# Kernel optimization log

Hardware: AMD Instinct MI355X
Metric: run time of the kernel (lower is better)

The kernel has to match this reference:

```python
import jax, jax.numpy as jnp
import numpy as np

N_UNITS = 100
N_INPUTS = 7
N_OUTPUTS = 1
T = 60
STIM_ON, STIM_OFF = 10, 15
RESP_START, RESP_END = 20, 35
REWARD_DURATION = 5
ALPHA = 0.2            # dt / tau = 100 / 500
SIGMA_REC = 0.15
B = 8192


def setup_inputs() -> dict:
    key = jax.random.key(0)
    k1, k2, k3, k4, k5, k6, k7 = jax.random.split(key, 7)
    W_in_raw = (jax.random.normal(k1, (N_UNITS, N_INPUTS)) * 0.05).astype(jnp.float32)
    W_rec_np = np.asarray(jax.random.normal(k2, (N_UNITS, N_UNITS))) / np.sqrt(N_UNITS)
    sr = float(np.abs(np.linalg.eigvals(W_rec_np)).max())
    W_rec = jnp.asarray(W_rec_np * (0.8 / sr), dtype=jnp.float32)
    b_rec = jnp.zeros((N_UNITS,), jnp.float32)
    w_out = (jax.random.normal(k3, (N_OUTPUTS, N_UNITS)) * 0.1).astype(jnp.float32)
    b_out = jnp.zeros((N_OUTPUTS,), jnp.float32)
    return {
        "y0": jnp.zeros((B, N_UNITS), jnp.float32),
        "noise": jax.random.normal(k4, (B, T, N_UNITS), dtype=jnp.float32),
        "stimulus_idx": jax.random.randint(k5, (B,), 0, 4).astype(jnp.int32),
        "rewarded_target_idx": jax.random.randint(k6, (B,), 0, 4).astype(jnp.int32),
        "instruction": jax.random.randint(k7, (B,), 0, 2).astype(jnp.int32),
        "W_in_raw": W_in_raw, "W_rec": W_rec, "b_rec": b_rec,
        "w_out": w_out, "b_out": b_out,
    }


def reference(y0, noise, stimulus_idx, rewarded_target_idx, instruction,
              W_in_raw, W_rec, b_rec, w_out, b_out):
    W_in = jnp.abs(W_in_raw)               # [N, n_in]
    w_lick = W_in[:, 5]
    w_reward = W_in[:, 4]
    noise_scale = SIGMA_REC * float(np.sqrt(2.0 * ALPHA))
    t_idx = jnp.arange(T, dtype=jnp.int32)
    stim_mask = ((t_idx >= STIM_ON) & (t_idx < STIM_OFF)).astype(jnp.float32)
    resp_mask = ((t_idx >= RESP_START) & (t_idx < RESP_END)).astype(jnp.float32)
    auto_start = RESP_END - REWARD_DURATION

    def trial(y0_i, eps_i, stim, rew, instr):
        is_rew = stim == rew
        instr_b = instr > 0
        # base open-loop input: stimulus channel + response cue (channel 6)
        u_base = jnp.zeros((T, N_INPUTS), jnp.float32).at[:, 6].set(resp_mask)
        u_base = u_base + stim_mask[:, None] * jax.nn.one_hot(stim, N_INPUTS, dtype=jnp.float32)
        wu = u_base @ W_in.T + b_rec        # [T, N]

        def step(carry, xs):
            y, licked, lick_t, instr_fired = carry
            t, wu_t, eps_t = xs
            # instruction auto-reward fires at auto_start if no reward yet (applied BEFORE pre)
            delivered = instr_fired | (licked & is_rew)
            fire = instr_b & (~delivered) & (t == auto_start)
            instr_fired = instr_fired | fire
            instr_active = instr_fired & (t >= auto_start) & (t < RESP_END)
            # lick-triggered inputs affect dynamics only AFTER the lick step (wu[t] already consumed)
            lick_dyn = licked & (t > lick_t) & (t < lick_t + REWARD_DURATION)
            add = (instr_active.astype(jnp.float32) + (lick_dyn & is_rew).astype(jnp.float32)) * w_reward \
                  + lick_dyn.astype(jnp.float32) * w_lick
            pre = y @ W_rec.T + wu_t + add + noise_scale * eps_t
            y = (1.0 - ALPHA) * y + ALPHA * jax.nn.relu(pre)
            z = jax.nn.sigmoid(y @ w_out.T + b_out)[0]
            # closed-loop lick decision (after readout)
            in_resp = (t >= RESP_START) & (t < RESP_END)
            trig = in_resp & (~licked) & (z > 0.5)
            lick_t = jnp.where(trig, t, lick_t)
            licked = licked | trig
            # u_trial markings include the lick step itself
            u5 = licked & (t >= lick_t) & (t < lick_t + REWARD_DURATION)
            u4 = instr_active | (u5 & is_rew)
            return (y, licked, lick_t, instr_fired), (z, u5, u4)

        init = (y0_i, jnp.array(False), jnp.array(T + 1, jnp.int32), jnp.array(False))
        (yf, licked, lick_t, instr_fired), (z_seq, u5, u4) = jax.lax.scan(
            step, init, (t_idx, wu, eps_i))
        u = u_base.at[:, 5].set(u5.astype(jnp.float32)).at[:, 4].set(u4.astype(jnp.float32))
        reward_delivered = instr_fired | (licked & is_rew)
        target = jnp.where(is_rew, resp_mask, jnp.zeros_like(resp_mask))
        return u, target, resp_mask > 0, licked, reward_delivered, z_seq, yf

    return jax.vmap(trial)(y0, noise, stimulus_idx, rewarded_target_idx, instruction)
```

## Files before the change

kernel.cpp:

```cpp
#include <hip/hip_runtime.h>
#include <math.h>

#define BB 8192
#define TT 60
#define NU 100
#define NI 7

typedef float v2f __attribute__((ext_vector_type(2)));

#define FOR50(M) M(0) M(1) M(2) M(3) M(4) M(5) M(6) M(7) M(8) M(9) \
  M(10) M(11) M(12) M(13) M(14) M(15) M(16) M(17) M(18) M(19) \
  M(20) M(21) M(22) M(23) M(24) M(25) M(26) M(27) M(28) M(29) \
  M(30) M(31) M(32) M(33) M(34) M(35) M(36) M(37) M(38) M(39) \
  M(40) M(41) M(42) M(43) M(44) M(45) M(46) M(47) M(48) M(49)

#define DECLW(sl) \
  const v2f wA_##sl = { W_rec[uao + 2*(sl)],     W_rec[ubo + 2*(sl)]     }; \
  const v2f wB_##sl = { W_rec[uao + 2*(sl) + 1], W_rec[ubo + 2*(sl) + 1] };

#define RL(v,l) __int_as_float(__builtin_amdgcn_readlane(__float_as_int(v), l))

#define MAC(sl) { \
  const float ya = RL(yy.x, sl); \
  const float yb = RL(yy.y, sl); \
  if ((sl) & 1) { accB0 += ya * wA_##sl; accB1 += yb * wB_##sl; } \
  else          { accA0 += ya * wA_##sl; accA1 += yb * wB_##sl; } }

#define DPPADD(ctrl, rmask) { \
  const int _t = __builtin_amdgcn_update_dpp(0, __float_as_int(part), (ctrl), (rmask), 0xf, false); \
  part += __int_as_float(_t); }

__global__ __launch_bounds__(256, 1)
void drr_kernel(const float* __restrict__ y0,
                const float* __restrict__ noise,
                const int*   __restrict__ stim_idx,
                const int*   __restrict__ rew_idx,
                const int*   __restrict__ instr_in,
                const float* __restrict__ W_in_raw,
                const float* __restrict__ W_rec,
                const float* __restrict__ b_rec,
                const float* __restrict__ w_out,
                const float* __restrict__ b_out,
                float* __restrict__ out)
{
    const int lane  = threadIdx.x & 63;
    const int wid   = threadIdx.x >> 6;
    const int trial = blockIdx.x * 4 + wid;

    const bool act = (lane < 50);
    const int  la  = act ? lane : 49;
    const int  ua  = 2 * la;
    const int  uao = ua * NU;
    const int  ubo = uao + NU;

    const int  stim    = stim_idx[trial];
    const int  rew     = rew_idx[trial];
    const bool is_rew  = (stim == rew);
    const bool instr_b = (instr_in[trial] > 0);

    FOR50(DECLW)

    const v2f wi6 = { fabsf(W_in_raw[ua * NI + 6]),    fabsf(W_in_raw[(ua+1) * NI + 6]) };
    const v2f wis = { fabsf(W_in_raw[ua * NI + stim]), fabsf(W_in_raw[(ua+1) * NI + stim]) };
    const v2f wr  = { fabsf(W_in_raw[ua * NI + 4]),    fabsf(W_in_raw[(ua+1) * NI + 4]) };
    const v2f wl  = { fabsf(W_in_raw[ua * NI + 5]),    fabsf(W_in_raw[(ua+1) * NI + 5]) };
    const v2f br  = { b_rec[ua], b_rec[ua + 1] };
    const v2f wo  = act ? (v2f){ w_out[ua], w_out[ua + 1] } : (v2f){ 0.0f, 0.0f };
    const float bo = b_out[0];

    const v2f* y0v = (const v2f*)(y0 + trial * NU);
    v2f yy = y0v[la];

    const float NS = 0.09486832980505138f;

    bool licked = false, instr_fired = false;
    int  lick_t = TT + 1;

    const float* nbase = noise + trial * (TT * NU);
    v2f en = ((const v2f*)nbase)[la];

    float* uout  = out;
    float* tout  = out  + BB * TT * NI;
    float* rout  = tout + BB * TT;
    float* lout  = rout + BB * TT;
    float* dout  = lout + BB;
    float* zout  = dout + BB;
    float* yfout = zout + BB * TT;

    for (int t = 0; t < TT; ++t) {
        const v2f e = en;
        if (t < TT - 1)
            en = ((const v2f*)(nbase + (t + 1) * NU))[la];

        const float sm = (t >= 10 && t < 15) ? 1.0f : 0.0f;
        const float rm = (t >= 20 && t < 35) ? 1.0f : 0.0f;

        const bool delivered    = instr_fired || (licked && is_rew);
        const bool fire         = instr_b && !delivered && (t == 30);
        instr_fired             = instr_fired || fire;
        const bool instr_active = instr_fired && (t >= 30) && (t < 35);
        const bool lick_dyn     = licked && (t > lick_t) && (t < lick_t + 5);
        const float a_rew  = (instr_active ? 1.0f : 0.0f) + ((lick_dyn && is_rew) ? 1.0f : 0.0f);
        const float a_lick = lick_dyn ? 1.0f : 0.0f;

        v2f accA0 = br + rm * wi6 + sm * wis + a_rew * wr + a_lick * wl + NS * e;
        v2f accA1 = { 0.0f, 0.0f };
        v2f accB0 = { 0.0f, 0.0f };
        v2f accB1 = { 0.0f, 0.0f };

        FOR50(MAC)

        const v2f pre = (accA0 + accA1) + (accB0 + accB1);
        const v2f prer = { fmaxf(pre.x, 0.0f), fmaxf(pre.y, 0.0f) };
        yy = 0.8f * yy + 0.2f * prer;

        float part = yy.x * wo.x + yy.y * wo.y;
        DPPADD(0x111, 0xf)
        DPPADD(0x112, 0xf)
        DPPADD(0x114, 0xf)
        DPPADD(0x118, 0xf)
        DPPADD(0x142, 0xa)
        DPPADD(0x143, 0xc)
        const float x = RL(part, 63) + bo;
        const float z = 1.0f / (1.0f + expf(-x));

        const bool in_resp = (t >= 20) && (t < 35);
        const bool trig    = in_resp && !licked && (z > 0.5f);
        if (trig) lick_t = t;
        licked = licked || trig;
        const bool u5 = licked && (t >= lick_t) && (t < lick_t + 5);
        const bool u4 = instr_active || (u5 && is_rew);

        const int bt = trial * TT + t;
        if (lane < NI) {
            float uv = 0.0f;
            if (lane == stim) uv = sm;
            if (lane == 4)    uv = u4 ? 1.0f : 0.0f;
            if (lane == 5)    uv = u5 ? 1.0f : 0.0f;
            if (lane == 6)    uv = rm;
            uout[bt * NI + lane] = uv;
        } else if (lane == 8) {
            tout[bt] = is_rew ? rm : 0.0f;
        } else if (lane == 9) {
            rout[bt] = rm;
        } else if (lane == 10) {
            zout[bt] = z;
        }
    }

    if (lane == 0) {
        lout[trial] = licked ? 1.0f : 0.0f;
        dout[trial] = (instr_fired || (licked && is_rew)) ? 1.0f : 0.0f;
    }
    if (act)
        ((v2f*)(yfout + trial * NU))[la] = yy;
}

extern "C" void kernel_launch(void* const* d_in, const int* in_sizes, int n_in,
                              void* d_out, int out_size, void* d_ws, size_t ws_size,
                              hipStream_t stream) {
    const float* y0       = (const float*)d_in[0];
    const float* noise    = (const float*)d_in[1];
    const int*   stim     = (const int*)  d_in[2];
    const int*   rew      = (const int*)  d_in[3];
    const int*   instr    = (const int*)  d_in[4];
    const float* W_in_raw = (const float*)d_in[5];
    const float* W_rec    = (const float*)d_in[6];
    const float* b_rec    = (const float*)d_in[7];
    const float* w_out    = (const float*)d_in[8];
    const float* b_out    = (const float*)d_in[9];
    float* out = (float*)d_out;

    drr_kernel<<<BB / 4, 256, 0, stream>>>(y0, noise, stim, rew, instr,
                                           W_in_raw, W_rec, b_rec, w_out, b_out, out);
}
```

Measured before the change: 585.8 us.

## Split recurrent matvec across block waves via LDS partial sums

Each of the four waves in a block now holds a 28-column slice of W_rec and computes partial matvec contributions for all four trials in the block, reading hidden states from LDS instead of broadcasting them with readlane. Partial sums are exchanged through LDS and combined by the owning wave, with two block-wide barriers per timestep. This cuts the per-thread weight register footprint so launch bounds can allow three blocks per CU, trading readlane-serialised work for LDS traffic and synchronisation.

```diff
diff --git a/kernel.cpp b/kernel.cpp
--- a/kernel.cpp
+++ b/kernel.cpp
@@ -7,30 +7,17 @@
 #define NI 7
 
 typedef float v2f __attribute__((ext_vector_type(2)));
-
-#define FOR50(M) M(0) M(1) M(2) M(3) M(4) M(5) M(6) M(7) M(8) M(9) \
-  M(10) M(11) M(12) M(13) M(14) M(15) M(16) M(17) M(18) M(19) \
-  M(20) M(21) M(22) M(23) M(24) M(25) M(26) M(27) M(28) M(29) \
-  M(30) M(31) M(32) M(33) M(34) M(35) M(36) M(37) M(38) M(39) \
-  M(40) M(41) M(42) M(43) M(44) M(45) M(46) M(47) M(48) M(49)
-
-#define DECLW(sl) \
-  const v2f wA_##sl = { W_rec[uao + 2*(sl)],     W_rec[ubo + 2*(sl)]     }; \
-  const v2f wB_##sl = { W_rec[uao + 2*(sl) + 1], W_rec[ubo + 2*(sl) + 1] };
-
+typedef float v4f __attribute__((ext_vector_type(4)));
+
+
+#define KEEP(x) asm volatile("" : "+v"(x))
 #define RL(v,l) __int_as_float(__builtin_amdgcn_readlane(__float_as_int(v), l))
-
-#define MAC(sl) { \
-  const float ya = RL(yy.x, sl); \
-  const float yb = RL(yy.y, sl); \
-  if ((sl) & 1) { accB0 += ya * wA_##sl; accB1 += yb * wB_##sl; } \
-  else          { accA0 += ya * wA_##sl; accA1 += yb * wB_##sl; } }
 
 #define DPPADD(ctrl, rmask) { \
   const int _t = __builtin_amdgcn_update_dpp(0, __float_as_int(part), (ctrl), (rmask), 0xf, false); \
   part += __int_as_float(_t); }
 
-__global__ __launch_bounds__(256, 1)
+__global__ __launch_bounds__(256, 3)
 void drr_kernel(const float* __restrict__ y0,
                 const float* __restrict__ noise,
                 const int*   __restrict__ stim_idx,
@@ -46,19 +33,31 @@
     const int lane  = threadIdx.x & 63;
     const int wid   = threadIdx.x >> 6;
     const int trial = blockIdx.x * 4 + wid;
+    const int kc    = wid * 28;
 
     const bool act = (lane < 50);
     const int  la  = act ? lane : 49;
     const int  ua  = 2 * la;
     const int  uao = ua * NU;
-    const int  ubo = uao + NU;
-
-    const int  stim    = stim_idx[trial];
-    const int  rew     = rew_idx[trial];
-    const bool is_rew  = (stim == rew);
-    const bool instr_b = (instr_in[trial] > 0);
-
-    FOR50(DECLW)
+
+    const int  stim   = stim_idx[trial];
+    const bool isrew  = (stim == rew_idx[trial]);
+    const bool instrb = (instr_in[trial] > 0);
+
+    v2f wa[14], wb[14];
+#pragma unroll
+    for (int p = 0; p < 14; ++p) {
+        const int k = kc + 2 * p;
+        if (k < NU) {
+            wa[p] = *(const v2f*)(W_rec + uao + k);
+            wb[p] = *(const v2f*)(W_rec + uao + NU + k);
+        } else {
+            wa[p] = (v2f){0.0f, 0.0f};
+            wb[p] = (v2f){0.0f, 0.0f};
+        }
+    }
+#pragma unroll
+    for (int p = 0; p < 14; ++p) { KEEP(wa[p]); KEEP(wb[p]); }
 
     const v2f wi6 = { fabsf(W_in_raw[ua * NI + 6]),    fabsf(W_in_raw[(ua+1) * NI + 6]) };
     const v2f wis = { fabsf(W_in_raw[ua * NI + stim]), fabsf(W_in_raw[(ua+1) * NI + stim]) };
@@ -68,16 +67,22 @@
     const v2f wo  = act ? (v2f){ w_out[ua], w_out[ua + 1] } : (v2f){ 0.0f, 0.0f };
     const float bo = b_out[0];
 
-    const v2f* y0v = (const v2f*)(y0 + trial * NU);
-    v2f yy = y0v[la];
+    v2f yy = ((const v2f*)(y0 + trial * NU))[la];
 
     const float NS = 0.09486832980505138f;
 
-    bool licked = false, instr_fired = false;
-    int  lick_t = TT + 1;
+    bool licked = false, fired = false;
+    int  lickt = TT + 1;
 
     const float* nbase = noise + trial * (TT * NU);
     v2f en = ((const v2f*)nbase)[la];
+
+    __shared__ v4f lds_y[4][28];
+    __shared__ v2f lds_p[4][4][64];
+
+    if (lane < 56)
+        ((v2f*)&lds_y[wid][0])[lane] = act ? yy : (v2f){0.0f, 0.0f};
+    __syncthreads();
 
     float* uout  = out;
     float* tout  = out  + BB * TT * NI;
@@ -87,32 +92,65 @@
     float* zout  = dout + BB;
     float* yfout = zout + BB * TT;
 
+    const v4f* Y0 = (const v4f*)&lds_y[0][0] + (kc >> 2);
+    const v4f* Y1 = (const v4f*)&lds_y[1][0] + (kc >> 2);
+    const v4f* Y2 = (const v4f*)&lds_y[2][0] + (kc >> 2);
+    const v4f* Y3 = (const v4f*)&lds_y[3][0] + (kc >> 2);
+
     for (int t = 0; t < TT; ++t) {
+        v2f a0A = {0,0}, a0B = {0,0}, a1A = {0,0}, a1B = {0,0};
+        v2f a2A = {0,0}, a2B = {0,0}, a3A = {0,0}, a3B = {0,0};
+#pragma unroll
+        for (int g = 0; g < 7; ++g) {
+            const v4f q0 = Y0[g];
+            const v4f q1 = Y1[g];
+            const v4f q2 = Y2[g];
+            const v4f q3 = Y3[g];
+            const v2f wA0 = wa[2*g], wA1 = wa[2*g+1];
+            const v2f wB0 = wb[2*g], wB1 = wb[2*g+1];
+            a0A += (v2f){q0.x,q0.y} * wA0;  a0A += (v2f){q0.z,q0.w} * wA1;
+            a0B += (v2f){q0.x,q0.y} * wB0;  a0B += (v2f){q0.z,q0.w} * wB1;
+            a1A += (v2f){q1.x,q1.y} * wA0;  a1A += (v2f){q1.z,q1.w} * wA1;
+            a1B += (v2f){q1.x,q1.y} * wB0;  a1B += (v2f){q1.z,q1.w} * wB1;
+            a2A += (v2f){q2.x,q2.y} * wA0;  a2A += (v2f){q2.z,q2.w} * wA1;
+            a2B += (v2f){q2.x,q2.y} * wB0;  a2B += (v2f){q2.z,q2.w} * wB1;
+            a3A += (v2f){q3.x,q3.y} * wA0;  a3A += (v2f){q3.z,q3.w} * wA1;
+            a3B += (v2f){q3.x,q3.y} * wB0;  a3B += (v2f){q3.z,q3.w} * wB1;
+        }
+
+        if (act) {
+            lds_p[0][wid][lane] = (v2f){ a0A.x + a0A.y, a0B.x + a0B.y };
+            lds_p[1][wid][lane] = (v2f){ a1A.x + a1A.y, a1B.x + a1B.y };
+            lds_p[2][wid][lane] = (v2f){ a2A.x + a2A.y, a2B.x + a2B.y };
+            lds_p[3][wid][lane] = (v2f){ a3A.x + a3A.y, a3B.x + a3B.y };
+        }
+        __syncthreads();
+
         const v2f e = en;
-        if (t < TT - 1)
-            en = ((const v2f*)(nbase + (t + 1) * NU))[la];
+        const int tn = (t < TT - 1) ? t + 1 : t;
+        en = ((const v2f*)(nbase + tn * NU))[la];
 
         const float sm = (t >= 10 && t < 15) ? 1.0f : 0.0f;
         const float rm = (t >= 20 && t < 35) ? 1.0f : 0.0f;
 
-        const bool delivered    = instr_fired || (licked && is_rew);
-        const bool fire         = instr_b && !delivered && (t == 30);
-        instr_fired             = instr_fired || fire;
-        const bool instr_active = instr_fired && (t >= 30) && (t < 35);
-        const bool lick_dyn     = licked && (t > lick_t) && (t < lick_t + 5);
-        const float a_rew  = (instr_active ? 1.0f : 0.0f) + ((lick_dyn && is_rew) ? 1.0f : 0.0f);
-        const float a_lick = lick_dyn ? 1.0f : 0.0f;
-
-        v2f accA0 = br + rm * wi6 + sm * wis + a_rew * wr + a_lick * wl + NS * e;
-        v2f accA1 = { 0.0f, 0.0f };
-        v2f accB0 = { 0.0f, 0.0f };
-        v2f accB1 = { 0.0f, 0.0f };
-
-        FOR50(MAC)
-
-        const v2f pre = (accA0 + accA1) + (accB0 + accB1);
+        const bool dl = fired || (licked && isrew);
+        const bool fr = instrb && !dl && (t == 30);
+        fired = fired || fr;
+        const bool ia = fired && (t >= 30) && (t < 35);
+        const bool ld = licked && (t > lickt) && (t < lickt + 5);
+        const float ar = (ia ? 1.0f : 0.0f) + ((ld && isrew) ? 1.0f : 0.0f);
+        const float al = ld ? 1.0f : 0.0f;
+        const v2f base = br + rm * wi6 + sm * wis + ar * wr + al * wl + NS * e;
+
+        const v2f psum = lds_p[wid][0][la] + lds_p[wid][1][la]
+                       + lds_p[wid][2][la] + lds_p[wid][3][la];
+        const v2f pre  = base + psum;
         const v2f prer = { fmaxf(pre.x, 0.0f), fmaxf(pre.y, 0.0f) };
         yy = 0.8f * yy + 0.2f * prer;
+
+        if (act)
+            ((v2f*)&lds_y[wid][0])[lane] = yy;
+        __syncthreads();
 
         float part = yy.x * wo.x + yy.y * wo.y;
         DPPADD(0x111, 0xf)
@@ -121,15 +159,15 @@
         DPPADD(0x118, 0xf)
         DPPADD(0x142, 0xa)
         DPPADD(0x143, 0xc)
-        const float x = RL(part, 63) + bo;
-        const float z = 1.0f / (1.0f + expf(-x));
-
-        const bool in_resp = (t >= 20) && (t < 35);
-        const bool trig    = in_resp && !licked && (z > 0.5f);
-        if (trig) lick_t = t;
+        const float xx = RL(part, 63) + bo;
+        const float z  = 1.0f / (1.0f + expf(-xx));
+
+        const bool inr  = (t >= 20) && (t < 35);
+        const bool trig = inr && !licked && (z > 0.5f);
+        if (trig) lickt = t;
         licked = licked || trig;
-        const bool u5 = licked && (t >= lick_t) && (t < lick_t + 5);
-        const bool u4 = instr_active || (u5 && is_rew);
+        const bool u5 = licked && (t >= lickt) && (t < lickt + 5);
+        const bool u4 = ia || (u5 && isrew);
 
         const int bt = trial * TT + t;
         if (lane < NI) {
@@ -140,7 +178,7 @@
             if (lane == 6)    uv = rm;
             uout[bt * NI + lane] = uv;
         } else if (lane == 8) {
-            tout[bt] = is_rew ? rm : 0.0f;
+            tout[bt] = isrew ? rm : 0.0f;
         } else if (lane == 9) {
             rout[bt] = rm;
         } else if (lane == 10) {
@@ -150,7 +188,7 @@
 
     if (lane == 0) {
         lout[trial] = licked ? 1.0f : 0.0f;
-        dout[trial] = (instr_fired || (licked && is_rew)) ? 1.0f : 0.0f;
+        dout[trial] = (fired || (licked && isrew)) ? 1.0f : 0.0f;
     }
     if (act)
         ((v2f*)(yfout + trial * NU))[la] = yy;
```

New measurement: 1.220 ms. +108.2%, slower.

## Batch four trials per wave with LDS-resident weights and LDS-broadcast state

Applied to the files above, without the earlier changes.

Each wave now advances four trials at once instead of one. W_rec is staged into shared memory in a transposed pair layout rather than held in per-lane registers. Each trial's hidden state is published to LDS every step and read back as vec4 broadcasts, replacing the 100 scalar readlanes per step. Each weight load from LDS then feeds four trials' FMAs, which cuts register pressure and the serial readlane chain. In exchange it adds LDS traffic each step and launches a quarter as many blocks, with launch bounds raised to allow two blocks per CU.

```diff
diff --git a/kernel.cpp b/kernel.cpp
--- a/kernel.cpp
+++ b/kernel.cpp
@@ -7,30 +7,93 @@
 #define NI 7
 
 typedef float v2f __attribute__((ext_vector_type(2)));
-
-#define FOR50(M) M(0) M(1) M(2) M(3) M(4) M(5) M(6) M(7) M(8) M(9) \
+typedef float v4f __attribute__((ext_vector_type(4)));
+
+
+#define FOR25(M) M(0) M(1) M(2) M(3) M(4) M(5) M(6) M(7) M(8) M(9) \
   M(10) M(11) M(12) M(13) M(14) M(15) M(16) M(17) M(18) M(19) \
-  M(20) M(21) M(22) M(23) M(24) M(25) M(26) M(27) M(28) M(29) \
-  M(30) M(31) M(32) M(33) M(34) M(35) M(36) M(37) M(38) M(39) \
-  M(40) M(41) M(42) M(43) M(44) M(45) M(46) M(47) M(48) M(49)
-
-#define DECLW(sl) \
-  const v2f wA_##sl = { W_rec[uao + 2*(sl)],     W_rec[ubo + 2*(sl)]     }; \
-  const v2f wB_##sl = { W_rec[uao + 2*(sl) + 1], W_rec[ubo + 2*(sl) + 1] };
+  M(20) M(21) M(22) M(23) M(24)
 
 #define RL(v,l) __int_as_float(__builtin_amdgcn_readlane(__float_as_int(v), l))
-
-#define MAC(sl) { \
-  const float ya = RL(yy.x, sl); \
-  const float yb = RL(yy.y, sl); \
-  if ((sl) & 1) { accB0 += ya * wA_##sl; accB1 += yb * wB_##sl; } \
-  else          { accA0 += ya * wA_##sl; accA1 += yb * wB_##sl; } }
 
 #define DPPADD(ctrl, rmask) { \
   const int _t = __builtin_amdgcn_update_dpp(0, __float_as_int(part), (ctrl), (rmask), 0xf, false); \
   part += __int_as_float(_t); }
 
-__global__ __launch_bounds__(256, 1)
+#define TRIAL_SETUP(s) \
+  const int  trial##s  = tbase + s; \
+  const int  stim##s   = stim_idx[trial##s]; \
+  const bool isrew##s  = (stim##s == rew_idx[trial##s]); \
+  const bool instrb##s = (instr_in[trial##s] > 0); \
+  const v2f  wis##s = { fabsf(W_in_raw[ua * NI + stim##s]), fabsf(W_in_raw[(ua+1) * NI + stim##s]) }; \
+  v2f  yy##s = ((const v2f*)(y0 + trial##s * NU))[la]; \
+  bool licked##s = false, fired##s = false; \
+  int  lickt##s = TT + 1; \
+  const float* nbase##s = noise + trial##s * (TT * NU); \
+  v2f  en##s = ((const v2f*)nbase##s)[la];
+
+#define PUBLISH(s) ((v2f*)&lds_y[wid * 4 + s][0])[la] = yy##s;
+
+#define DECLACC(s) v2f aX0_##s = {0,0}, aX1_##s = {0,0}, aY0_##s = {0,0}, aY1_##s = {0,0};
+
+#define MACQ(s, j2) { \
+  const v4f q = Y##s[j2]; \
+  aX0_##s += (v2f){q.x, q.y} * wx0; \
+  aY0_##s += (v2f){q.x, q.y} * wy0; \
+  aX1_##s += (v2f){q.z, q.w} * wx1; \
+  aY1_##s += (v2f){q.z, q.w} * wy1; }
+
+#define MACJ2(j2) { \
+  const v2f wx0 = wX[(2*(j2)    ) * 50 + la]; \
+  const v2f wx1 = wX[(2*(j2) + 1) * 50 + la]; \
+  const v2f wy0 = wY[(2*(j2)    ) * 50 + la]; \
+  const v2f wy1 = wY[(2*(j2) + 1) * 50 + la]; \
+  MACQ(0, j2) MACQ(1, j2) MACQ(2, j2) MACQ(3, j2) }
+
+#define TAILA(s, t, sm, rm) { \
+  const v2f e = en##s; \
+  en##s = ((const v2f*)(nbase##s + tn * NU))[la]; \
+  const bool dl = fired##s || (licked##s && isrew##s); \
+  const bool fr = instrb##s && !dl && ((t) == 30); \
+  fired##s = fired##s || fr; \
+  ia##s = fired##s && ((t) >= 30) && ((t) < 35); \
+  const bool ld = licked##s && ((t) > lickt##s) && ((t) < lickt##s + 5); \
+  const float ar = (ia##s ? 1.0f : 0.0f) + ((ld && isrew##s) ? 1.0f : 0.0f); \
+  const float al = ld ? 1.0f : 0.0f; \
+  const v2f base = br + (rm) * wi6 + (sm) * wis##s + ar * wr + al * wl + NS * e; \
+  const v2f sX = aX0_##s + aX1_##s; \
+  const v2f sY = aY0_##s + aY1_##s; \
+  const v2f pre  = base + (v2f){ sX.x + sX.y, sY.x + sY.y }; \
+  const v2f prer = { fmaxf(pre.x, 0.0f), fmaxf(pre.y, 0.0f) }; \
+  yy##s = 0.8f * yy##s + 0.2f * prer; }
+
+#define ZED(s, t) { \
+  float part = yy##s.x * wo.x + yy##s.y * wo.y; \
+  DPPADD(0x111, 0xf) DPPADD(0x112, 0xf) DPPADD(0x114, 0xf) DPPADD(0x118, 0xf) \
+  DPPADD(0x142, 0xa) DPPADD(0x143, 0xc) \
+  const float xx = RL(part, 63) + bo; \
+  z##s = 1.0f / (1.0f + expf(-xx)); \
+  const bool inr  = ((t) >= 20) && ((t) < 35); \
+  const bool trig = inr && !licked##s && (z##s > 0.5f); \
+  if (trig) lickt##s = (t); \
+  licked##s = licked##s || trig; \
+  u5##s = licked##s && ((t) >= lickt##s) && ((t) < lickt##s + 5); \
+  u4##s = ia##s || (u5##s && isrew##s); }
+
+#define FSTORE(s, t, sm, rm) { \
+  const int bt = trial##s * TT + (t); \
+  if (lane < NI) { \
+    float uv = 0.0f; \
+    if (lane == stim##s) uv = (sm); \
+    if (lane == 4) uv = u4##s ? 1.0f : 0.0f; \
+    if (lane == 5) uv = u5##s ? 1.0f : 0.0f; \
+    if (lane == 6) uv = (rm); \
+    uout[bt * NI + lane] = uv; \
+  } else if (lane == 8) { tout[bt] = isrew##s ? (rm) : 0.0f; } \
+  else if (lane == 9)   { rout[bt] = (rm); } \
+  else if (lane == 10)  { zout[bt] = z##s; } }
+
+__global__ __launch_bounds__(256, 2)
 void drr_kernel(const float* __restrict__ y0,
                 const float* __restrict__ noise,
                 const int*   __restrict__ stim_idx,
@@ -43,41 +106,40 @@
                 const float* __restrict__ b_out,
                 float* __restrict__ out)
 {
-    const int lane  = threadIdx.x & 63;
-    const int wid   = threadIdx.x >> 6;
-    const int trial = blockIdx.x * 4 + wid;
+    const int tid   = threadIdx.x;
+    const int lane  = tid & 63;
+    const int wid   = tid >> 6;
+    const int tbase = blockIdx.x * 16 + wid * 4;
 
     const bool act = (lane < 50);
     const int  la  = act ? lane : 49;
     const int  ua  = 2 * la;
-    const int  uao = ua * NU;
-    const int  ubo = uao + NU;
-
-    const int  stim    = stim_idx[trial];
-    const int  rew     = rew_idx[trial];
-    const bool is_rew  = (stim == rew);
-    const bool instr_b = (instr_in[trial] > 0);
-
-    FOR50(DECLW)
-
-    const v2f wi6 = { fabsf(W_in_raw[ua * NI + 6]),    fabsf(W_in_raw[(ua+1) * NI + 6]) };
-    const v2f wis = { fabsf(W_in_raw[ua * NI + stim]), fabsf(W_in_raw[(ua+1) * NI + stim]) };
-    const v2f wr  = { fabsf(W_in_raw[ua * NI + 4]),    fabsf(W_in_raw[(ua+1) * NI + 4]) };
-    const v2f wl  = { fabsf(W_in_raw[ua * NI + 5]),    fabsf(W_in_raw[(ua+1) * NI + 5]) };
+
+    __shared__ v2f wtX[2500];
+    __shared__ v2f wtY[2500];
+    __shared__ v4f lds_y[16][26];
+
+    for (int idx = tid; idx < 2500; idx += 256) {
+        const int j = idx / 50, l = idx % 50;
+        wtX[idx] = *(const v2f*)(W_rec + (2 * l)     * NU + 2 * j);
+        wtY[idx] = *(const v2f*)(W_rec + (2 * l + 1) * NU + 2 * j);
+    }
+    __syncthreads();
+
+    const v2f wi6 = { fabsf(W_in_raw[ua * NI + 6]), fabsf(W_in_raw[(ua+1) * NI + 6]) };
+    const v2f wr  = { fabsf(W_in_raw[ua * NI + 4]), fabsf(W_in_raw[(ua+1) * NI + 4]) };
+    const v2f wl  = { fabsf(W_in_raw[ua * NI + 5]), fabsf(W_in_raw[(ua+1) * NI + 5]) };
     const v2f br  = { b_rec[ua], b_rec[ua + 1] };
     const v2f wo  = act ? (v2f){ w_out[ua], w_out[ua + 1] } : (v2f){ 0.0f, 0.0f };
     const float bo = b_out[0];
-
-    const v2f* y0v = (const v2f*)(y0 + trial * NU);
-    v2f yy = y0v[la];
-
     const float NS = 0.09486832980505138f;
 
-    bool licked = false, instr_fired = false;
-    int  lick_t = TT + 1;
-
-    const float* nbase = noise + trial * (TT * NU);
-    v2f en = ((const v2f*)nbase)[la];
+    TRIAL_SETUP(0) TRIAL_SETUP(1) TRIAL_SETUP(2) TRIAL_SETUP(3)
+
+    const v4f* Y0 = &lds_y[wid * 4 + 0][0];
+    const v4f* Y1 = &lds_y[wid * 4 + 1][0];
+    const v4f* Y2 = &lds_y[wid * 4 + 2][0];
+    const v4f* Y3 = &lds_y[wid * 4 + 3][0];
 
     float* uout  = out;
     float* tout  = out  + BB * TT * NI;
@@ -88,72 +150,50 @@
     float* yfout = zout + BB * TT;
 
     for (int t = 0; t < TT; ++t) {
-        const v2f e = en;
-        if (t < TT - 1)
-            en = ((const v2f*)(nbase + (t + 1) * NU))[la];
-
+        unsigned wofs = 0;
+        asm volatile("" : "+v"(wofs));
+        const v2f* wX = (const v2f*)wtX + wofs;
+        const v2f* wY = (const v2f*)wtY + wofs;
+
+        PUBLISH(0) PUBLISH(1) PUBLISH(2) PUBLISH(3)
+
+        DECLACC(0) DECLACC(1) DECLACC(2) DECLACC(3)
+
+        FOR25(MACJ2)
+
+        const int tn = (t < TT - 1) ? t + 1 : t;
         const float sm = (t >= 10 && t < 15) ? 1.0f : 0.0f;
         const float rm = (t >= 20 && t < 35) ? 1.0f : 0.0f;
 
-        const bool delivered    = instr_fired || (licked && is_rew);
-        const bool fire         = instr_b && !delivered && (t == 30);
-        instr_fired             = instr_fired || fire;
-        const bool instr_active = instr_fired && (t >= 30) && (t < 35);
-        const bool lick_dyn     = licked && (t > lick_t) && (t < lick_t + 5);
-        const float a_rew  = (instr_active ? 1.0f : 0.0f) + ((lick_dyn && is_rew) ? 1.0f : 0.0f);
-        const float a_lick = lick_dyn ? 1.0f : 0.0f;
-
-        v2f accA0 = br + rm * wi6 + sm * wis + a_rew * wr + a_lick * wl + NS * e;
-        v2f accA1 = { 0.0f, 0.0f };
-        v2f accB0 = { 0.0f, 0.0f };
-        v2f accB1 = { 0.0f, 0.0f };
-
-        FOR50(MAC)
-
-        const v2f pre = (accA0 + accA1) + (accB0 + accB1);
-        const v2f prer = { fmaxf(pre.x, 0.0f), fmaxf(pre.y, 0.0f) };
-        yy = 0.8f * yy + 0.2f * prer;
-
-        float part = yy.x * wo.x + yy.y * wo.y;
-        DPPADD(0x111, 0xf)
-        DPPADD(0x112, 0xf)
-        DPPADD(0x114, 0xf)
-        DPPADD(0x118, 0xf)
-        DPPADD(0x142, 0xa)
-        DPPADD(0x143, 0xc)
-        const float x = RL(part, 63) + bo;
-        const float z = 1.0f / (1.0f + expf(-x));
-
-        const bool in_resp = (t >= 20) && (t < 35);
-        const bool trig    = in_resp && !licked && (z > 0.5f);
-        if (trig) lick_t = t;
-        licked = licked || trig;
-        const bool u5 = licked && (t >= lick_t) && (t < lick_t + 5);
-        const bool u4 = instr_active || (u5 && is_rew);
-
-        const int bt = trial * TT + t;
-        if (lane < NI) {
-            float uv = 0.0f;
-            if (lane == stim) uv = sm;
-            if (lane == 4)    uv = u4 ? 1.0f : 0.0f;
-            if (lane == 5)    uv = u5 ? 1.0f : 0.0f;
-            if (lane == 6)    uv = rm;
-            uout[bt * NI + lane] = uv;
-        } else if (lane == 8) {
-            tout[bt] = is_rew ? rm : 0.0f;
-        } else if (lane == 9) {
-            rout[bt] = rm;
-        } else if (lane == 10) {
-            zout[bt] = z;
-        }
+        bool ia0, ia1, ia2, ia3;
+        float z0, z1, z2, z3;
+        bool u40, u41, u42, u43, u50, u51, u52, u53;
+
+        TAILA(0, t, sm, rm) TAILA(1, t, sm, rm)
+        TAILA(2, t, sm, rm) TAILA(3, t, sm, rm)
+
+        ZED(0, t) ZED(1, t) ZED(2, t) ZED(3, t)
+
+        FSTORE(0, t, sm, rm) FSTORE(1, t, sm, rm)
+        FSTORE(2, t, sm, rm) FSTORE(3, t, sm, rm)
     }
 
     if (lane == 0) {
-        lout[trial] = licked ? 1.0f : 0.0f;
-        dout[trial] = (instr_fired || (licked && is_rew)) ? 1.0f : 0.0f;
-    }
-    if (act)
-        ((v2f*)(yfout + trial * NU))[la] = yy;
+        lout[trial0] = licked0 ? 1.0f : 0.0f;
+        dout[trial0] = (fired0 || (licked0 && isrew0)) ? 1.0f : 0.0f;
+        lout[trial1] = licked1 ? 1.0f : 0.0f;
+        dout[trial1] = (fired1 || (licked1 && isrew1)) ? 1.0f : 0.0f;
+        lout[trial2] = licked2 ? 1.0f : 0.0f;
+        dout[trial2] = (fired2 || (licked2 && isrew2)) ? 1.0f : 0.0f;
+        lout[trial3] = licked3 ? 1.0f : 0.0f;
+        dout[trial3] = (fired3 || (licked3 && isrew3)) ? 1.0f : 0.0f;
+    }
+    if (act) {
+        ((v2f*)(yfout + trial0 * NU))[la] = yy0;
+        ((v2f*)(yfout + trial1 * NU))[la] = yy1;
+        ((v2f*)(yfout + trial2 * NU))[la] = yy2;
+        ((v2f*)(yfout + trial3 * NU))[la] = yy3;
+    }
 }
 
 extern "C" void kernel_launch(void* const* d_in, const int* in_sizes, int n_in,
@@ -171,6 +211,6 @@
     const float* b_out    = (const float*)d_in[9];
     float* out = (float*)d_out;
 
-    drr_kernel<<<BB / 4, 256, 0, stream>>>(y0, noise, stim, rew, instr,
-                                           W_in_raw, W_rec, b_rec, w_out, b_out, out);
+    drr_kernel<<<BB / 16, 256, 0, stream>>>(y0, noise, stim, rew, instr,
+                                            W_in_raw, W_rec, b_rec, w_out, b_out, out);
 }
```

Result: faster. 508.4 us (-13.2%).
